# Optimization experiments

Hardware: AMD Instinct MI355X
Metric: run time of the kernel (lower is better)

## Reference

```python
import jax, jax.numpy as jnp
import numpy as np

EPS = 1e-5
FIXED = 6  # attention_dim


def _layernorm(x, g, b):
    mu = x.mean(-1, keepdims=True)
    var = ((x - mu) ** 2).mean(-1, keepdims=True)
    return (x - mu) * jax.lax.rsqrt(var + EPS) * g + b


def _mha(x, Wqkv, bqkv, Wo, bo, num_heads):
    # x: [B,S,D]; torch nn.MultiheadAttention (batch_first), attn weights averaged over heads
    B, S, D = x.shape
    hd = D // num_heads
    qkv = x @ Wqkv.T + bqkv                      # [B,S,3D]
    q, k, v = jnp.split(qkv, 3, axis=-1)
    sh = lambda t: t.reshape(B, S, num_heads, hd).transpose(0, 2, 1, 3)  # [B,H,S,hd]
    q, k, v = sh(q), sh(k), sh(v)
    scores = jnp.einsum('bhqd,bhkd->bhqk', q, k) / np.sqrt(hd).astype(np.float32)
    attn = jax.nn.softmax(scores, axis=-1)
    out = jnp.einsum('bhqk,bhkd->bhqd', attn, v).transpose(0, 2, 1, 3).reshape(B, S, D)
    return out @ Wo.T + bo, attn.mean(axis=1)    # [B,S,D], [B,S,S]


def _gcn(x, edge_index, W, b):
    # PyG GCNConv: add self-loops, symmetric normalization, aggregate into dst
    N = x.shape[0]
    loop = jnp.arange(N, dtype=edge_index.dtype)
    src = jnp.concatenate([edge_index[0], loop])
    dst = jnp.concatenate([edge_index[1], loop])
    deg = jax.ops.segment_sum(jnp.ones(src.shape[0], x.dtype), dst, num_segments=N)
    dinv = jax.lax.rsqrt(jnp.maximum(deg, 1.0))  # deg >= 1 with self-loops
    norm = dinv[src] * dinv[dst]                 # [E+N]
    h = x @ W.T                                  # [N,D]
    msg = h[src] * norm[:, None]
    return jax.ops.segment_sum(msg, dst, num_segments=N) + b


def setup_inputs() -> dict:
    key = jax.random.key(0)
    ks = jax.random.split(key, 24)
    D = 768
    N, E, U, K, B, S = 100000, 1600000, 1024, 32, 8, 126
    w = lambda k, shp: jax.random.normal(k, shp, jnp.float32) * 0.02
    return {
        'user_text': jax.random.normal(ks[0], (B, S, D), jnp.float32),
        'all_user_feature': jax.random.normal(ks[1], (N, D), jnp.float32),
        'user_neighbor_index': jax.random.randint(ks[2], (U, K), 0, N),
        'edge_index': jax.random.randint(ks[3], (2, E), 0, N),
        # LModel (text transformer block) params
        'Wqkv_l': w(ks[4], (3 * D, D)), 'bqkv_l': jnp.zeros((3 * D,), jnp.float32),
        'Wo_l': w(ks[5], (D, D)), 'bo_l': jnp.zeros((D,), jnp.float32),
        'ln1_g': jnp.ones((D,), jnp.float32), 'ln1_b': jnp.zeros((D,), jnp.float32),
        'ln2_g': jnp.ones((D,), jnp.float32), 'ln2_b': jnp.zeros((D,), jnp.float32),
        'W1': w(ks[6], (D, D)), 'b1': jnp.zeros((D,), jnp.float32),
        'W2': w(ks[7], (D, D)), 'b2': jnp.zeros((D,), jnp.float32),
        # GCNConv params
        'Wg': w(ks[8], (D, D)), 'bg': jnp.zeros((D,), jnp.float32),
        # MultiAttn (per-neighborhood attention) params
        'Wqkv_m': w(ks[9], (3 * D, D)), 'bqkv_m': jnp.zeros((3 * D,), jnp.float32),
        'Wo_m': w(ks[10], (D, D)), 'bo_m': jnp.zeros((D,), jnp.float32),
    }


def reference(user_text, all_user_feature, user_neighbor_index, edge_index,
              Wqkv_l, bqkv_l, Wo_l, bo_l, ln1_g, ln1_b, ln2_g, ln2_b,
              W1, b1, W2, b2, Wg, bg, Wqkv_m, bqkv_m, Wo_m, bo_m):
    # --- LModel: pre-norm transformer block (dropout = eval identity) ---
    sa, attn_w = _mha(_layernorm(user_text, ln1_g, ln1_b), Wqkv_l, bqkv_l, Wo_l, bo_l, 4)
    text = user_text + sa
    h = jax.nn.leaky_relu(_layernorm(text, ln2_g, ln2_b) @ W1.T + b1)  # LeakyReLU(0.01)
    text = text + (h @ W2.T + b2)

    # --- GCN over the user graph (NeighborSampler sizes=[-1] == full 1-hop) ---
    feats = _gcn(all_user_feature, edge_index, Wg, bg)

    # --- MultiAttn: self-attention within each neighborhood, write back center ---
    nb = feats[user_neighbor_index]                       # [U,K,D] gather
    nb_out, _ = _mha(nb, Wqkv_m, bqkv_m, Wo_m, bo_m, 4)   # batched over U
    feats = feats.at[user_neighbor_index[:, 0]].set(nb_out[:, 0, :])

    # --- FixedPooling: adaptive avg-pool attention map [B,S,S] -> [B,6,6] ---
    B, S, _ = attn_w.shape
    p = S // FIXED
    attention_graph = attn_w.reshape(B, FIXED, p, FIXED, p).mean(axis=(2, 4))
    return text, feats, attention_graph
```

## Files before the change

kernel.cpp:

```cpp
#include <hip/hip_runtime.h>
#include <stdint.h>

typedef __attribute__((ext_vector_type(8))) short short8;
typedef __attribute__((ext_vector_type(4))) float f32x4;

__device__ __forceinline__ float bf2f(uint16_t u) {
    union { uint32_t i; float f; } v; v.i = ((uint32_t)u) << 16; return v.f;
}
__device__ __forceinline__ uint16_t f2bf(float f) {
    union { float f; uint32_t i; } v; v.f = f;
    uint32_t r = v.i + 0x7fffu + ((v.i >> 16) & 1u);
    return (uint16_t)(r >> 16);
}
__device__ __forceinline__ short8 cvt8(const float* p) {
    f32x4 a = *(const f32x4*)p;
    f32x4 b = *(const f32x4*)(p + 4);
    short8 r;
    r[0] = (short)f2bf(a[0]); r[1] = (short)f2bf(a[1]);
    r[2] = (short)f2bf(a[2]); r[3] = (short)f2bf(a[3]);
    r[4] = (short)f2bf(b[0]); r[5] = (short)f2bf(b[1]);
    r[6] = (short)f2bf(b[2]); r[7] = (short)f2bf(b[3]);
    return r;
}

__global__ void code_write_f32(float* __restrict__ out, int n, float codef)
{
    int i = blockIdx.x * 256 + threadIdx.x;
    if (i < n) out[i] = codef;
}

__global__ __launch_bounds__(256) void gemm_bt(
    const float* __restrict__ A, const float* __restrict__ W,
    const float* __restrict__ bias, void* __restrict__ Cv,
    const float* __restrict__ R, const int* __restrict__ rowmap, int rstride,
    int M, int N, int act, int cbf)
{
    __shared__ __attribute__((aligned(16))) uint16_t As[4096];
    __shared__ __attribute__((aligned(16))) uint16_t Ws[4096];
    const int K = 768;
    int tid = threadIdx.x, wv = tid >> 6, ln = tid & 63;
    int bn = blockIdx.x, bm = blockIdx.y;
    int wm = wv >> 1, wn = wv & 1;

    const f32x4 zero4 = {0.f, 0.f, 0.f, 0.f};
    f32x4 acc[4][4];
#pragma unroll
    for (int i = 0; i < 4; ++i)
#pragma unroll
        for (int j = 0; j < 4; ++j) acc[i][j] = zero4;

    int r0 = tid >> 2, cb = tid & 3;
    int c8 = cb * 8;
    int r1 = r0 + 64;
    int ar0 = min(bm * 128 + r0, M - 1);
    int ar1 = min(bm * 128 + r1, M - 1);
    if (rowmap) { ar0 = rowmap[(size_t)ar0 * rstride]; ar1 = rowmap[(size_t)ar1 * rstride]; }
    int br0 = bn * 128 + r0, br1 = bn * 128 + r1;
    const float* Af0 = A + (size_t)ar0 * K + c8;
    const float* Af1 = A + (size_t)ar1 * K + c8;
    const float* Wf0 = W + (size_t)br0 * K + c8;
    const float* Wf1 = W + (size_t)br1 * K + c8;
    const int sw  = (cb ^ (r0 & 3)) * 8;
    const int s0 = r0 * 32 + sw;
    const int s1 = 2048 + r0 * 32 + sw;
    const int lr = ln & 15, kg = ln >> 4;
    const int kgsw = (kg ^ (lr & 3)) * 8;

    for (int k0 = 0; k0 < K; k0 += 32) {
        short8 a0 = cvt8(Af0 + k0);
        short8 a1 = cvt8(Af1 + k0);
        short8 w0 = cvt8(Wf0 + k0);
        short8 w1 = cvt8(Wf1 + k0);
        __syncthreads();
        *(short8*)&As[s0] = a0;
        *(short8*)&As[s1] = a1;
        *(short8*)&Ws[s0] = w0;
        *(short8*)&Ws[s1] = w1;
        __syncthreads();
        short8 afr[4], bfr[4];
#pragma unroll
        for (int mi = 0; mi < 4; ++mi)
            afr[mi] = *(const short8*)&As[(wm * 64 + mi * 16 + lr) * 32 + kgsw];
#pragma unroll
        for (int nj = 0; nj < 4; ++nj)
            bfr[nj] = *(const short8*)&Ws[(wn * 64 + nj * 16 + lr) * 32 + kgsw];
#pragma unroll
        for (int mi = 0; mi < 4; ++mi)
#pragma unroll
            for (int nj = 0; nj < 4; ++nj)
                acc[mi][nj] = __builtin_amdgcn_mfma_f32_16x16x32_bf16(
                    afr[mi], bfr[nj], acc[mi][nj], 0, 0, 0);
    }

#pragma unroll
    for (int mi = 0; mi < 4; ++mi) {
        int growb = bm * 128 + wm * 64 + mi * 16 + kg * 4;
#pragma unroll
        for (int nj = 0; nj < 4; ++nj) {
            int gcol = bn * 128 + wn * 64 + nj * 16 + lr;
            float bs = bias ? bias[gcol] : 0.f;
#pragma unroll
            for (int q = 0; q < 4; ++q) {
                int grow = growb + q;
                if (grow < M) {
                    float val = acc[mi][nj][q] + bs;
                    if (R) val += R[(size_t)grow * N + gcol];
                    if (act == 1) val = (val > 0.f) ? val : 0.01f * val;
                    size_t idx = (size_t)grow * N + gcol;
                    if (cbf) ((uint16_t*)Cv)[idx] = f2bf(val);
                    else     ((float*)Cv)[idx]    = val;
                }
            }
        }
    }
}

__global__ __launch_bounds__(256) void ln_kernel(
    const float* __restrict__ x, const float* __restrict__ g,
    const float* __restrict__ bb, float* __restrict__ y)
{
    int row = blockIdx.x, tid = threadIdx.x;
    const float* xr = x + (size_t)row * 768;
    float v0 = xr[tid], v1 = xr[tid + 256], v2 = xr[tid + 512];
    float s = v0 + v1 + v2;
    __shared__ float red[4];
#pragma unroll
    for (int mk = 32; mk >= 1; mk >>= 1) s += __shfl_xor(s, mk);
    int wv = tid >> 6, ln = tid & 63;
    if (ln == 0) red[wv] = s;
    __syncthreads();
    float mu = (red[0] + red[1] + red[2] + red[3]) * (1.f / 768.f);
    float d0 = v0 - mu, d1 = v1 - mu, d2 = v2 - mu;
    float ss = d0 * d0 + d1 * d1 + d2 * d2;
#pragma unroll
    for (int mk = 32; mk >= 1; mk >>= 1) ss += __shfl_xor(ss, mk);
    __syncthreads();
    if (ln == 0) red[wv] = ss;
    __syncthreads();
    float var = (red[0] + red[1] + red[2] + red[3]) * (1.f / 768.f);
    float inv = 1.0f / sqrtf(var + 1e-5f);
    float* yr = y + (size_t)row * 768;
    yr[tid]       = d0 * inv * g[tid]       + bb[tid];
    yr[tid + 256] = d1 * inv * g[tid + 256] + bb[tid + 256];
    yr[tid + 512] = d2 * inv * g[tid + 512] + bb[tid + 512];
}

__global__ __launch_bounds__(256) void nattn(
    const float* __restrict__ qkv, float* __restrict__ attnout,
    float* __restrict__ pooled)
{
    int b = blockIdx.x / 126, i = blockIdx.x % 126;
    int tid = threadIdx.x;
    __shared__ float P[4][128];
    __shared__ float poolloc[6];
    if (tid < 6) poolloc[tid] = 0.f;
    const size_t base = (size_t)b * 126 * 2304;
    const float scale = 0.0721687836f;

    for (int p = tid; p < 504; p += 256) {
        int h = p / 126, j = p - h * 126;
        const float* qr = qkv + base + (size_t)i * 2304 + h * 192;
        const float* kr = qkv + base + (size_t)j * 2304 + 768 + h * 192;
        float a = 0.f;
#pragma unroll 8
        for (int d = 0; d < 192; ++d) a += qr[d] * kr[d];
        P[h][j] = a * scale;
    }
    __syncthreads();

    {
        int w = tid >> 6, ln = tid & 63;
        bool v1 = (ln + 64) < 126;
        float s0 = P[w][ln];
        float s1 = v1 ? P[w][ln + 64] : -1e30f;
        float m = fmaxf(s0, s1);
#pragma unroll
        for (int mk = 32; mk >= 1; mk >>= 1) m = fmaxf(m, __shfl_xor(m, mk));
        float e0 = __expf(s0 - m);
        float e1 = v1 ? __expf(s1 - m) : 0.f;
        float z = e0 + e1;
#pragma unroll
        for (int mk = 32; mk >= 1; mk >>= 1) z += __shfl_xor(z, mk);
        float rz = 1.f / z;
        P[w][ln] = e0 * rz;
        if (v1) P[w][ln + 64] = e1 * rz;
    }
    __syncthreads();

    if (tid < 126) {
        float s4 = P[0][tid] + P[1][tid] + P[2][tid] + P[3][tid];
        atomicAdd(&poolloc[tid / 21], s4);
    }

    float o[3];
#pragma unroll
    for (int r = 0; r < 3; ++r) {
        int od = tid + r * 256;
        int h = od / 192;
        float a = 0.f;
        for (int j = 0; j < 126; ++j)
            a += P[h][j] * qkv[base + (size_t)j * 2304 + 1536 + od];
        o[r] = a;
    }
    float* orow = attnout + (size_t)(b * 126 + i) * 768;
#pragma unroll
    for (int r = 0; r < 3; ++r) orow[tid + r * 256] = o[r];

    __syncthreads();
    if (tid < 6)
        atomicAdd(&pooled[b * 36 + (i / 21) * 6 + tid], poolloc[tid]);
}

__global__ void pool_fin_kernel(const float* __restrict__ pooled, float* __restrict__ outp)
{
    int i = blockIdx.x * 36 + threadIdx.x;
    outp[i] = pooled[i] * (1.0f / 1764.0f);
}

__global__ void deg_fill_kernel(const int* __restrict__ ei, int E,
                                int* __restrict__ cnt, int* __restrict__ bucket)
{
    int e = blockIdx.x * 256 + threadIdx.x;
    if (e < E) {
        int s = ei[e], d = ei[E + e];
        int p = atomicAdd(&cnt[d], 1);
        if (p < 64) bucket[(size_t)d * 64 + p] = s;
    }
}
__global__ void dinv_kernel(const int* __restrict__ cnt, float* __restrict__ ds, int N)
{
    int i = blockIdx.x * 256 + threadIdx.x;
    if (i < N) ds[i] = 1.0f / sqrtf((float)cnt[i] + 1.0f);
}

__global__ __launch_bounds__(256) void gcn_agg(
    const uint16_t* __restrict__ h, const int* __restrict__ bucket,
    const int* __restrict__ cnt, const float* __restrict__ dsc,
    const float* __restrict__ bg, float* __restrict__ feats)
{
    int v = blockIdx.x;
    int tid = threadIdx.x;
    __shared__ int nbs[64];
    int nb = min(cnt[v], 64);
    if (tid < nb)
        nbs[tid] = __builtin_nontemporal_load(&bucket[(size_t)v * 64 + tid]);
    __syncthreads();
    const uint16_t* hv = h + (size_t)v * 768;
    float sv = dsc[v];
    float a0 = bf2f(hv[tid]) * sv, a1 = bf2f(hv[tid + 256]) * sv, a2 = bf2f(hv[tid + 512]) * sv;
    for (int e = 0; e < nb; ++e) {
        int s = nbs[e];
        const uint16_t* hs = h + (size_t)s * 768;
        float ss = dsc[s];
        a0 += bf2f(hs[tid]) * ss; a1 += bf2f(hs[tid + 256]) * ss; a2 += bf2f(hs[tid + 512]) * ss;
    }
    float* o = feats + (size_t)v * 768;
    __builtin_nontemporal_store(a0 * sv + bg[tid],       &o[tid]);
    __builtin_nontemporal_store(a1 * sv + bg[tid + 256], &o[tid + 256]);
    __builtin_nontemporal_store(a2 * sv + bg[tid + 512], &o[tid + 512]);
}

__global__ __launch_bounds__(256) void attn_m_kernel(
    const float* __restrict__ kv, const float* __restrict__ qc,
    float* __restrict__ out0)
{
    int u = blockIdx.x;
    int tid = threadIdx.x, h = tid >> 6, ln = tid & 63;
    const float scale = 0.0721687836f;
    float s = -1e30f;
    {
        int j = (ln < 32) ? ln : 0;
        const float* qr = qc + (size_t)u * 768 + h * 192;
        const float* kr = kv + ((size_t)u * 32 + j) * 1536 + h * 192;
        float a = 0.f;
#pragma unroll 8
        for (int d = 0; d < 192; ++d) a += qr[d] * kr[d];
        if (ln < 32) s = a * scale;
    }
    float m = s;
#pragma unroll
    for (int mk = 32; mk >= 1; mk >>= 1) m = fmaxf(m, __shfl_xor(m, mk));
    float e = (ln < 32) ? __expf(s - m) : 0.f;
    float z = e;
#pragma unroll
    for (int mk = 32; mk >= 1; mk >>= 1) z += __shfl_xor(z, mk);
    __shared__ float pbuf[4][32];
    if (ln < 32) pbuf[h][ln] = e / z;
    __syncthreads();
    float a0 = 0.f, a1 = 0.f, a2 = 0.f;
    for (int j = 0; j < 32; ++j) {
        const float* vr = kv + ((size_t)u * 32 + j) * 1536 + 768 + h * 192;
        float p = pbuf[h][j];
        a0 += p * vr[ln]; a1 += p * vr[ln + 64]; a2 += p * vr[ln + 128];
    }
    float* o = out0 + (size_t)u * 768 + h * 192;
    o[ln] = a0; o[ln + 64] = a1; o[ln + 128] = a2;
}

__global__ void winner_kernel(const int* __restrict__ nbidx, int* __restrict__ slot, int U)
{
    int u = blockIdx.x * 256 + threadIdx.x;
    if (u < U) atomicMax(&slot[nbidx[(size_t)u * 32]], u);
}
__global__ __launch_bounds__(256) void scatter_kernel(
    const float* __restrict__ proj, const int* __restrict__ nbidx,
    const int* __restrict__ slot, float* __restrict__ feats)
{
    int u = blockIdx.x;
    int c = nbidx[(size_t)u * 32];
    if (slot[c] != u) return;
    const float* src = proj + (size_t)u * 768;
    float* dst = feats + (size_t)c * 768;
    for (int t = threadIdx.x; t < 768; t += 256) dst[t] = src[t];
}

extern "C" void kernel_launch(void* const* d_in, const int* in_sizes, int n_in,
                              void* d_out, int out_size, void* d_ws, size_t ws_size,
                              hipStream_t stream)
{
    const float* user_text = (const float*)d_in[0];
    const float* auf       = (const float*)d_in[1];
    const int*   nbidx     = (const int*)d_in[2];
    const int*   ei        = (const int*)d_in[3];
    const float* Wqkv_l = (const float*)d_in[4];
    const float* bqkv_l = (const float*)d_in[5];
    const float* Wo_l   = (const float*)d_in[6];
    const float* bo_l   = (const float*)d_in[7];
    const float* ln1_g  = (const float*)d_in[8];
    const float* ln1_b  = (const float*)d_in[9];
    const float* ln2_g  = (const float*)d_in[10];
    const float* ln2_b  = (const float*)d_in[11];
    const float* W1 = (const float*)d_in[12];
    const float* b1 = (const float*)d_in[13];
    const float* W2 = (const float*)d_in[14];
    const float* b2 = (const float*)d_in[15];
    const float* Wg = (const float*)d_in[16];
    const float* bg = (const float*)d_in[17];
    const float* Wqkv_m = (const float*)d_in[18];
    const float* bqkv_m = (const float*)d_in[19];
    const float* Wo_m   = (const float*)d_in[20];
    const float* bo_m   = (const float*)d_in[21];

    const int D  = 768;
    const int BS = in_sizes[0] / D;
    const int B  = BS / 126;
    const int N  = in_sizes[1] / D;
    const int U  = in_sizes[2] / 32;
    const int E  = in_sizes[3] / 2;
    const int UK = U * 32;

    float* out_text  = (float*)d_out;
    const int TEXTN = BS * D;
    const int WG_T = (TEXTN + 255) / 256;
    float* out_feats = out_text + (size_t)TEXTN;
    float* out_pool  = out_feats + (size_t)N * D;

    char* ws = (char*)d_ws;
    size_t off = 0;
    auto take = [&](size_t bytes) -> void* {
        void* p = ws + off;
        off += (bytes + 255) & ~(size_t)255;
        return p;
    };
    float* A_h    = (float*)take((size_t)N * D * 4);
    float* qkvl   = (float*)take((size_t)BS * 2304 * 4);
    float* ln1x   = (float*)take((size_t)BS * D * 4);
    float* attnout= (float*)take((size_t)BS * D * 4);
    float* text1  = (float*)take((size_t)BS * D * 4);
    float* ln2x   = (float*)take((size_t)BS * D * 4);
    float* qc     = (float*)take((size_t)U * D * 4);
    float* out0   = (float*)take((size_t)U * D * 4);
    float* projm  = (float*)take((size_t)U * D * 4);
    int*   cnt    = (int*)take((size_t)N * 4);
    float* dsc    = (float*)take((size_t)N * 4);
    int*   slot   = (int*)take((size_t)N * 4);
    int*   bucket = (int*)take((size_t)N * 64 * 4);
    float* pooled = (float*)take((size_t)B * 36 * 4);
    float* hmid   = ln1x;
    uint16_t* hbf = (uint16_t*)A_h;
    float* kv     = A_h;
    size_t required = off;

    if (ws_size < required) {
        code_write_f32<<<WG_T, 256, 0, stream>>>(out_text, TEXTN,
            1.0e6f + (float)(ws_size >> 20) * 1000.0f);
        return;
    }

    hipMemsetAsync(cnt, 0, (size_t)N * 4, stream);
    hipMemsetAsync(slot, 0xFF, (size_t)N * 4, stream);
    hipMemsetAsync(pooled, 0, (size_t)B * 36 * 4, stream);

    deg_fill_kernel<<<(E + 255) / 256, 256, 0, stream>>>(ei, E, cnt, bucket);
    dinv_kernel<<<(N + 255) / 256, 256, 0, stream>>>(cnt, dsc, N);

    const int BMT = (BS + 127) / 128;
    ln_kernel<<<BS, 256, 0, stream>>>(user_text, ln1_g, ln1_b, ln1x);
    gemm_bt<<<dim3(18, BMT), 256, 0, stream>>>(
        ln1x, Wqkv_l, bqkv_l, qkvl, nullptr, nullptr, 1, BS, 2304, 0, 0);
    nattn<<<BS, 256, 0, stream>>>(qkvl, attnout, pooled);
    gemm_bt<<<dim3(6, BMT), 256, 0, stream>>>(
        attnout, Wo_l, bo_l, text1, user_text, nullptr, 1, BS, 768, 0, 0);
    ln_kernel<<<BS, 256, 0, stream>>>(text1, ln2_g, ln2_b, ln2x);
    gemm_bt<<<dim3(6, BMT), 256, 0, stream>>>(
        ln2x, W1, b1, hmid, nullptr, nullptr, 1, BS, 768, 1, 0);
    gemm_bt<<<dim3(6, BMT), 256, 0, stream>>>(
        hmid, W2, b2, out_text, text1, nullptr, 1, BS, 768, 0, 0);
    pool_fin_kernel<<<B, 36, 0, stream>>>(pooled, out_pool);

    gemm_bt<<<dim3(6, (N + 127) / 128), 256, 0, stream>>>(
        auf, Wg, nullptr, hbf, nullptr, nullptr, 1, N, 768, 0, 1);
    gcn_agg<<<N, 256, 0, stream>>>(hbf, bucket, cnt, dsc, bg, out_feats);

    winner_kernel<<<(U + 255) / 256, 256, 0, stream>>>(nbidx, slot, U);
    gemm_bt<<<dim3(12, UK / 128), 256, 0, stream>>>(
        out_feats, Wqkv_m + (size_t)768 * 768, bqkv_m + 768, kv, nullptr, nbidx, 1, UK, 1536, 0, 0);
    gemm_bt<<<dim3(6, U / 128), 256, 0, stream>>>(
        out_feats, Wqkv_m, bqkv_m, qc, nullptr, nbidx, 32, U, 768, 0, 0);
    attn_m_kernel<<<U, 256, 0, stream>>>(kv, qc, out0);
    gemm_bt<<<dim3(6, U / 128), 256, 0, stream>>>(
        out0, Wo_m, bo_m, projm, nullptr, nullptr, 1, U, 768, 0, 0);
    scatter_kernel<<<U, 256, 0, stream>>>(projm, nbidx, slot, out_feats);
}
```

Before: 1.596 ms.

## Remap GEMM blocks to XCD-contiguous row ranges and use packed bf16 conversion

The GEMM grid becomes 1D, and block IDs are remapped so that each of the 8 dispatch groups (round-robin XCDs on MI355X) handles a contiguous range of M-tiles across all N-tiles. The goal is better L2 reuse of A rows within each XCD. Separately, the float-to-bf16 conversion in the A/W load path now uses the HIP packed __float22bfloat162_rn intrinsic instead of manual rounding. The remap pads the grid with blocks that exit early, and assumes N is a multiple of 128.

After: 1.548 ms. -3.0%, faster.

```diff
diff --git a/kernel.cpp b/kernel.cpp
--- a/kernel.cpp
+++ b/kernel.cpp
@@ -1,4 +1,5 @@
 #include <hip/hip_runtime.h>
+#include <hip/hip_bf16.h>
 #include <stdint.h>
 
 typedef __attribute__((ext_vector_type(8))) short short8;
@@ -13,14 +14,13 @@
     return (uint16_t)(r >> 16);
 }
 __device__ __forceinline__ short8 cvt8(const float* p) {
-    f32x4 a = *(const f32x4*)p;
-    f32x4 b = *(const f32x4*)(p + 4);
-    short8 r;
-    r[0] = (short)f2bf(a[0]); r[1] = (short)f2bf(a[1]);
-    r[2] = (short)f2bf(a[2]); r[3] = (short)f2bf(a[3]);
-    r[4] = (short)f2bf(b[0]); r[5] = (short)f2bf(b[1]);
-    r[6] = (short)f2bf(b[2]); r[7] = (short)f2bf(b[3]);
-    return r;
+    const float2* f2 = (const float2*)p;
+    union { __hip_bfloat162 h[4]; short8 s; } c;
+    c.h[0] = __float22bfloat162_rn(f2[0]);
+    c.h[1] = __float22bfloat162_rn(f2[1]);
+    c.h[2] = __float22bfloat162_rn(f2[2]);
+    c.h[3] = __float22bfloat162_rn(f2[3]);
+    return c.s;
 }
 
 __global__ void code_write_f32(float* __restrict__ out, int n, float codef)
@@ -35,11 +35,20 @@
     const float* __restrict__ R, const int* __restrict__ rowmap, int rstride,
     int M, int N, int act, int cbf)
 {
+    const int K = 768;
+    int numN = N >> 7;
+    int numM = (M + 127) >> 7;
+    int lid = blockIdx.x;
+    int x = lid & 7, j = lid >> 3;
+    int bm_local = j / numN, bn = j - bm_local * numN;
+    int q = numM >> 3, rr = numM & 7;
+    int cnt = q + (x < rr ? 1 : 0);
+    if (bm_local >= cnt) return;
+    int bm = x * q + min(x, rr) + bm_local;
+
     __shared__ __attribute__((aligned(16))) uint16_t As[4096];
     __shared__ __attribute__((aligned(16))) uint16_t Ws[4096];
-    const int K = 768;
     int tid = threadIdx.x, wv = tid >> 6, ln = tid & 63;
-    int bn = blockIdx.x, bm = blockIdx.y;
     int wm = wv >> 1, wn = wv & 1;
 
     const f32x4 zero4 = {0.f, 0.f, 0.f, 0.f};
@@ -47,7 +56,7 @@
 #pragma unroll
     for (int i = 0; i < 4; ++i)
 #pragma unroll
-        for (int j = 0; j < 4; ++j) acc[i][j] = zero4;
+        for (int jj = 0; jj < 4; ++jj) acc[i][jj] = zero4;
 
     int r0 = tid >> 2, cb = tid & 3;
     int c8 = cb * 8;
@@ -100,10 +109,10 @@
             int gcol = bn * 128 + wn * 64 + nj * 16 + lr;
             float bs = bias ? bias[gcol] : 0.f;
 #pragma unroll
-            for (int q = 0; q < 4; ++q) {
-                int grow = growb + q;
+            for (int qq = 0; qq < 4; ++qq) {
+                int grow = growb + qq;
                 if (grow < M) {
-                    float val = acc[mi][nj][q] + bs;
+                    float val = acc[mi][nj][qq] + bs;
                     if (R) val += R[(size_t)grow * N + gcol];
                     if (act == 1) val = (val > 0.f) ? val : 0.01f * val;
                     size_t idx = (size_t)grow * N + gcol;
@@ -312,6 +321,11 @@
     const float* src = proj + (size_t)u * 768;
     float* dst = feats + (size_t)c * 768;
     for (int t = threadIdx.x; t < 768; t += 256) dst[t] = src[t];
+}
+
+static inline int gemm_blocks(int M, int N) {
+    int numM = (M + 127) >> 7, numN = N >> 7;
+    return 8 * ((numM + 7) / 8) * numN;
 }
 
 extern "C" void kernel_launch(void* const* d_in, const int* in_sizes, int n_in,
@@ -394,31 +408,30 @@
     deg_fill_kernel<<<(E + 255) / 256, 256, 0, stream>>>(ei, E, cnt, bucket);
     dinv_kernel<<<(N + 255) / 256, 256, 0, stream>>>(cnt, dsc, N);
 
-    const int BMT = (BS + 127) / 128;
     ln_kernel<<<BS, 256, 0, stream>>>(user_text, ln1_g, ln1_b, ln1x);
-    gemm_bt<<<dim3(18, BMT), 256, 0, stream>>>(
+    gemm_bt<<<gemm_blocks(BS, 2304), 256, 0, stream>>>(
         ln1x, Wqkv_l, bqkv_l, qkvl, nullptr, nullptr, 1, BS, 2304, 0, 0);
     nattn<<<BS, 256, 0, stream>>>(qkvl, attnout, pooled);
-    gemm_bt<<<dim3(6, BMT), 256, 0, stream>>>(
+    gemm_bt<<<gemm_blocks(BS, 768), 256, 0, stream>>>(
         attnout, Wo_l, bo_l, text1, user_text, nullptr, 1, BS, 768, 0, 0);
     ln_kernel<<<BS, 256, 0, stream>>>(text1, ln2_g, ln2_b, ln2x);
-    gemm_bt<<<dim3(6, BMT), 256, 0, stream>>>(
+    gemm_bt<<<gemm_blocks(BS, 768), 256, 0, stream>>>(
         ln2x, W1, b1, hmid, nullptr, nullptr, 1, BS, 768, 1, 0);
-    gemm_bt<<<dim3(6, BMT), 256, 0, stream>>>(
+    gemm_bt<<<gemm_blocks(BS, 768), 256, 0, stream>>>(
         hmid, W2, b2, out_text, text1, nullptr, 1, BS, 768, 0, 0);
     pool_fin_kernel<<<B, 36, 0, stream>>>(pooled, out_pool);
 
-    gemm_bt<<<dim3(6, (N + 127) / 128), 256, 0, stream>>>(
+    gemm_bt<<<gemm_blocks(N, 768), 256, 0, stream>>>(
         auf, Wg, nullptr, hbf, nullptr, nullptr, 1, N, 768, 0, 1);
     gcn_agg<<<N, 256, 0, stream>>>(hbf, bucket, cnt, dsc, bg, out_feats);
 
     winner_kernel<<<(U + 255) / 256, 256, 0, stream>>>(nbidx, slot, U);
-    gemm_bt<<<dim3(12, UK / 128), 256, 0, stream>>>(
+    gemm_bt<<<gemm_blocks(UK, 1536), 256, 0, stream>>>(
         out_feats, Wqkv_m + (size_t)768 * 768, bqkv_m + 768, kv, nullptr, nbidx, 1, UK, 1536, 0, 0);
-    gemm_bt<<<dim3(6, U / 128), 256, 0, stream>>>(
+    gemm_bt<<<gemm_blocks(U, 768), 256, 0, stream>>>(
         out_feats, Wqkv_m, bqkv_m, qc, nullptr, nbidx, 32, U, 768, 0, 0);
     attn_m_kernel<<<U, 256, 0, stream>>>(kv, qc, out0);
-    gemm_bt<<<dim3(6, U / 128), 256, 0, stream>>>(
+    gemm_bt<<<gemm_blocks(U, 768), 256, 0, stream>>>(
         out0, Wo_m, bo_m, projm, nullptr, nullptr, 1, U, 768, 0, 0);
     scatter_kernel<<<U, 256, 0, stream>>>(projm, nbidx, slot, out_feats);
 }
```
